# Optimization experiments

Hardware: AMD Instinct MI355X
Metric: run time of the kernel (lower is better)

The kernel has to match this reference:

```python
import jax, jax.numpy as jnp
import numpy as np
from functools import partial

WS = 11          # window size (safe for H=W=256)
SIGMA = 1.5
DATA_RANGE = 1.0
EPS = 1e-8


def _gaussian_window(ws: int, sigma: float, channels: int) -> jnp.ndarray:
    coords = jnp.arange(ws, dtype=jnp.float32) - ws // 2
    g = jnp.exp(-(coords ** 2) / (2.0 * sigma * sigma))
    g = g / (g.sum() + 1e-12)
    win2d = jnp.outer(g, g)                      # [ws, ws]
    # depthwise kernel: OIHW with O=C, I=1, feature_group_count=C
    return jnp.broadcast_to(win2d, (channels, 1, ws, ws))


def _depthwise_conv(x: jnp.ndarray, win: jnp.ndarray) -> jnp.ndarray:
    # x: [N, C, H, W]; same-padding depthwise Gaussian filter
    c = x.shape[1]
    pad = WS // 2
    return jax.lax.conv_general_dilated(
        x, win,
        window_strides=(1, 1),
        padding=[(pad, pad), (pad, pad)],
        dimension_numbers=('NCHW', 'OIHW', 'NCHW'),
        feature_group_count=c,
    )


def setup_inputs() -> dict:
    key = jax.random.key(0)
    k1, k2 = jax.random.split(key)
    shape = (8, 8, 3, 256, 256)  # [B, T, C, H, W]
    pred = jax.random.uniform(k1, shape, dtype=jnp.float32)
    target = jax.random.uniform(k2, shape, dtype=jnp.float32)
    return {"pred": pred, "target": target}


def reference(pred, target):
    pred = jnp.clip(pred.astype(jnp.float32), 0.0, 1.0)
    target = jnp.clip(target.astype(jnp.float32), 0.0, 1.0)
    B, T, C, H, W = pred.shape
    x = pred.reshape(B * T, C, H, W)
    y = target.reshape(B * T, C, H, W)

    win = _gaussian_window(WS, SIGMA, C)

    mu_x = _depthwise_conv(x, win)
    mu_y = _depthwise_conv(y, win)
    mu_x2 = mu_x * mu_x
    mu_y2 = mu_y * mu_y
    mu_xy = mu_x * mu_y

    sigma_x2 = jnp.maximum(_depthwise_conv(x * x, win) - mu_x2, 0.0)
    sigma_y2 = jnp.maximum(_depthwise_conv(y * y, win) - mu_y2, 0.0)
    sigma_xy = _depthwise_conv(x * y, win) - mu_xy

    C1 = (0.01 * DATA_RANGE) ** 2
    C2 = (0.03 * DATA_RANGE) ** 2
    num = (2.0 * mu_xy + C1) * (2.0 * sigma_xy + C2)
    den = (mu_x2 + mu_y2 + C1) * (sigma_x2 + sigma_y2 + C2)
    ssim_map = num / (den + EPS)
    ssim_map = jnp.nan_to_num(ssim_map, nan=0.0, posinf=0.0, neginf=0.0)
    return 1.0 - jnp.mean(ssim_map)
```

## Files before the change

kernel.cpp:

```cpp
#include <hip/hip_runtime.h>


typedef _Float16 h2 __attribute__((ext_vector_type(2)));
typedef __fp16 fp16v2 __attribute__((ext_vector_type(2)));

#define WSZ 11
#define RAD 5
#define IMH 256
#define IMW 256
#define BROWS 16
#define HROWS (BROWS + 2 * RAD)
#define NBANDS (IMH / BROWS)
#define NPLANES 192
#define NGRID (NPLANES * NBANDS)
#define WPB 4
#define RPW (BROWS / WPB)
#define NPIXF (192.0f * 256.0f * 256.0f)

#define GW0 0.001028381f
#define GW1 0.007598770f
#define GW2 0.036000770f
#define GW3 0.109360600f
#define GW4 0.213005700f
#define GW5 0.266011790f

__device__ __forceinline__ h2 pk_fma16(h2 a, h2 b, h2 c) {
    h2 d;
    asm("v_pk_fma_f16 %0, %1, %2, %3" : "=v"(d) : "v"(a), "v"(b), "v"(c));
    return d;
}
__device__ __forceinline__ h2 pk_mul16(h2 a, h2 b) {
    h2 d;
    asm("v_pk_mul_f16 %0, %1, %2" : "=v"(d) : "v"(a), "v"(b));
    return d;
}
__device__ __forceinline__ h2 pk_add16(h2 a, h2 b) {
    h2 d;
    asm("v_pk_add_f16 %0, %1, %2" : "=v"(d) : "v"(a), "v"(b));
    return d;
}
__device__ __forceinline__ h2 pk_min16(h2 a, h2 b) {
    h2 d;
    asm("v_pk_min_f16 %0, %1, %2" : "=v"(d) : "v"(a), "v"(b));
    return d;
}
__device__ __forceinline__ h2 pk_max16(h2 a, h2 b) {
    h2 d;
    asm("v_pk_max_f16 %0, %1, %2" : "=v"(d) : "v"(a), "v"(b));
    return d;
}

union H2U { h2 h; unsigned u; };
__device__ __forceinline__ unsigned h2u(h2 v) { H2U x; x.h = v; return x.u; }
__device__ __forceinline__ h2 u2h(unsigned v) { H2U x; x.u = v; return x.h; }

__device__ __forceinline__ h2 bperm(int idx, h2 v) {
    return u2h((unsigned)__builtin_amdgcn_ds_bpermute(idx, (int)h2u(v)));
}
__device__ __forceinline__ h2 albt(h2 hi, h2 lo) {
    return u2h(__builtin_amdgcn_alignbit(h2u(hi), h2u(lo), 16));
}

__device__ __forceinline__ h2 splat16(float s) {
    _Float16 t = (_Float16)s;
    return (h2){t, t};
}
__device__ __forceinline__ h2 zero16() { return (h2){(_Float16)0, (_Float16)0}; }

__device__ __forceinline__ h2 clip_pack(float a, float b, h2 Z, h2 O) {
    fp16v2 r = __builtin_amdgcn_cvt_pkrtz(a, b);
    h2 v = __builtin_bit_cast(h2, r);
    return pk_min16(pk_max16(v, Z), O);
}

__global__ __launch_bounds__(256, 4) void ssim_band_kernel(
    const float* __restrict__ pred,
    const float* __restrict__ targ,
    float* __restrict__ partial)
{
    const int tid = threadIdx.x;
    const int lane = tid & 63;
    const int wid = tid >> 6;
    const int blk = blockIdx.x;
    const int plane = blk >> 4;
    const int band = blk & 15;
    const int r0 = band * BROWS;

    const float4* __restrict__ pp =
        (const float4*)(pred + (size_t)plane * (IMH * IMW));
    const float4* __restrict__ tp =
        (const float4*)(targ + (size_t)plane * (IMH * IMW));

    const h2 W0 = splat16(GW0), W1 = splat16(GW1), W2 = splat16(GW2),
             W3 = splat16(GW3), W4 = splat16(GW4), W5 = splat16(GW5);
    const h2 wv16[WSZ] = {W0, W1, W2, W3, W4, W5, W4, W3, W2, W1, W0};
    const h2 M2 = splat16(-2.0f);
    const h2 Z16 = zero16();
    const h2 O16 = splat16(1.0f);

    __shared__ uint4 lds[HROWS * 64];
    __shared__ float wsum[WPB];

    for (int j = wid; j < HROWS; j += WPB) {
        const int r = r0 - RAD + j;
        const int rc = min(max(r, 0), IMH - 1);
        const bool oob = (r < 0) | (r >= IMH);
        const float4 a = pp[rc * 64 + lane];
        const float4 c = tp[rc * 64 + lane];
        const h2 x0 = clip_pack(a.x, a.y, Z16, O16);
        const h2 x1 = clip_pack(a.z, a.w, Z16, O16);
        const h2 y0 = clip_pack(c.x, c.y, Z16, O16);
        const h2 y1 = clip_pack(c.z, c.w, Z16, O16);
        const h2 s0 = pk_add16(x0, y0);
        const h2 s1 = pk_add16(x1, y1);
        const h2 d0 = pk_fma16(M2, y0, s0);
        const h2 d1 = pk_fma16(M2, y1, s1);
        uint4 w;
        w.x = oob ? 0u : h2u(s0);
        w.y = oob ? 0u : h2u(d0);
        w.z = oob ? 0u : h2u(s1);
        w.w = oob ? 0u : h2u(d1);
        lds[j * 64 + lane] = w;
    }
    __syncthreads();

    const int iu1 = (lane - 1) << 2;
    const int iu2 = (lane - 2) << 2;
    const int id1 = (lane + 1) << 2;
    const int id2 = (lane + 2) << 2;
    const bool mu1 = lane >= 1;
    const bool mu2 = lane >= 2;
    const bool md1 = lane <= 62;
    const bool md2 = lane <= 61;

    const float C1 = 1e-4f, C2 = 9e-4f;
    float lsum = 0.f;

#pragma unroll
    for (int i = 0; i < RPW; ++i) {
        const int jb = wid * RPW + i;

        h2 vd[4][2];
#pragma unroll
        for (int p = 0; p < 2; ++p) {
            vd[0][p] = zero16(); vd[1][p] = zero16();
            vd[2][p] = zero16(); vd[3][p] = zero16();
        }
#pragma unroll
        for (int k = 0; k < WSZ; ++k) {
            const uint4 v = lds[(jb + k) * 64 + lane];
            const h2 wk = wv16[k];
            const h2 sA = u2h(v.x), dA = u2h(v.y);
            const h2 sB = u2h(v.z), dB = u2h(v.w);
            h2 ws = pk_mul16(wk, sA);
            h2 wd = pk_mul16(wk, dA);
            vd[0][0] = pk_add16(vd[0][0], ws);
            vd[1][0] = pk_add16(vd[1][0], wd);
            vd[2][0] = pk_fma16(ws, sA, vd[2][0]);
            vd[3][0] = pk_fma16(wd, dA, vd[3][0]);
            ws = pk_mul16(wk, sB);
            wd = pk_mul16(wk, dB);
            vd[0][1] = pk_add16(vd[0][1], ws);
            vd[1][1] = pk_add16(vd[1][1], wd);
            vd[2][1] = pk_fma16(ws, sB, vd[2][1]);
            vd[3][1] = pk_fma16(wd, dB, vd[3][1]);
        }

        h2 hf[4][2];
#pragma unroll
        for (int ch = 0; ch < 4; ++ch) {
            const h2 H0 = vd[ch][0], H1 = vd[ch][1];
            h2 Gm3 = bperm(iu2, H1);
            h2 Gm2 = bperm(iu1, H0);
            h2 Gm1 = bperm(iu1, H1);
            h2 G2  = bperm(id1, H0);
            h2 G3  = bperm(id1, H1);
            h2 G4  = bperm(id2, H0);
            Gm3 = mu2 ? Gm3 : zero16();
            Gm2 = mu1 ? Gm2 : zero16();
            Gm1 = mu1 ? Gm1 : zero16();
            G2  = md1 ? G2  : zero16();
            G3  = md1 ? G3  : zero16();
            G4  = md2 ? G4  : zero16();
            const h2 P0  = albt(Gm2, Gm3);
            const h2 P1  = Gm2;
            const h2 P2  = albt(Gm1, Gm2);
            const h2 P3  = Gm1;
            const h2 P4  = albt(H0, Gm1);
            const h2 P5  = H0;
            const h2 P6  = albt(H1, H0);
            const h2 P7  = H1;
            const h2 P8  = albt(G2, H1);
            const h2 P9  = G2;
            const h2 P10 = albt(G3, G2);
            const h2 P11 = G3;
            const h2 P12 = albt(G4, G3);
            h2 a0 = pk_mul16(W0, P0);
            a0 = pk_fma16(W1, P1, a0);
            a0 = pk_fma16(W2, P2, a0);
            a0 = pk_fma16(W3, P3, a0);
            a0 = pk_fma16(W4, P4, a0);
            a0 = pk_fma16(W5, P5, a0);
            a0 = pk_fma16(W4, P6, a0);
            a0 = pk_fma16(W3, P7, a0);
            a0 = pk_fma16(W2, P8, a0);
            a0 = pk_fma16(W1, P9, a0);
            a0 = pk_fma16(W0, P10, a0);
            h2 a1 = pk_mul16(W0, P2);
            a1 = pk_fma16(W1, P3, a1);
            a1 = pk_fma16(W2, P4, a1);
            a1 = pk_fma16(W3, P5, a1);
            a1 = pk_fma16(W4, P6, a1);
            a1 = pk_fma16(W5, P7, a1);
            a1 = pk_fma16(W4, P8, a1);
            a1 = pk_fma16(W3, P9, a1);
            a1 = pk_fma16(W2, P10, a1);
            a1 = pk_fma16(W1, P11, a1);
            a1 = pk_fma16(W0, P12, a1);
            hf[ch][0] = a0;
            hf[ch][1] = a1;
        }

#pragma unroll
        for (int p = 0; p < 2; ++p) {
#pragma unroll
            for (int e = 0; e < 2; ++e) {
                const float ms = (float)hf[0][p][e];
                const float md = (float)hf[1][p][e];
                const float Ss = (float)hf[2][p][e];
                const float Sd = (float)hf[3][p][e];
                const float P = ms * ms, Q = md * md;
                const float mxy2 = 0.5f * (P - Q);
                const float m2s  = 0.5f * (P + Q);
                const float Ssum = 0.5f * (Ss + Sd);
                const float ssum = fmaxf(Ssum - m2s, 0.f);
                const float sxy2 = fmaf(0.5f, Ss - Sd, -mxy2);
                const float num = (mxy2 + C1) * (sxy2 + C2);
                const float den = fmaf(m2s + C1, ssum + C2, 1e-8f);
                lsum += num * __builtin_amdgcn_rcpf(den);
            }
        }
    }

#pragma unroll
    for (int off = 32; off > 0; off >>= 1)
        lsum += __shfl_xor(lsum, off, 64);

    if (lane == 0) wsum[wid] = lsum;
    __syncthreads();
    if (tid == 0)
        partial[blk] = wsum[0] + wsum[1] + wsum[2] + wsum[3];
}

__global__ __launch_bounds__(256) void ssim_finalize(
    const float* __restrict__ partial,
    float* __restrict__ out)
{
    __shared__ float wsum[4];
    const int t = threadIdx.x;
    float s = 0.f;
    for (int i = t; i < NGRID; i += 256) s += partial[i];
#pragma unroll
    for (int off = 32; off > 0; off >>= 1)
        s += __shfl_xor(s, off, 64);
    const int lane = t & 63, wv = t >> 6;
    if (lane == 0) wsum[wv] = s;
    __syncthreads();
    if (t == 0)
        out[0] = 1.0f - (wsum[0] + wsum[1] + wsum[2] + wsum[3]) / NPIXF;
}

extern "C" void kernel_launch(void* const* d_in, const int* in_sizes, int n_in,
                              void* d_out, int out_size, void* d_ws, size_t ws_size,
                              hipStream_t stream) {
    const float* pred = (const float*)d_in[0];
    const float* targ = (const float*)d_in[1];
    float* out = (float*)d_out;
    float* part = (float*)d_ws;

    ssim_band_kernel<<<NGRID, 256, 0, stream>>>(pred, targ, part);
    ssim_finalize<<<1, 256, 0, stream>>>(part, out);
}
```

Before: 142.5 us.

## Compute separable Gaussian convolutions with MFMA banded-matrix multiplies

Replaces the packed-FP16 vertical and horizontal 11-tap filters with 16x16x32 f16 MFMA operations against a banded Gaussian weight matrix generated per lane. Input rows are clipped, converted to sum/difference form and stored transposed in LDS. A vertical MFMA pass follows, its results are written back to LDS with zero padding, and a horizontal MFMA pass produces the four statistics. This moves the FMA-heavy stencil work from VALU onto matrix cores, at the cost of redundant zero multiplications, extra LDS traffic and transposes, and an additional barrier.

```diff
diff --git a/kernel.cpp b/kernel.cpp
--- a/kernel.cpp
+++ b/kernel.cpp
@@ -2,6 +2,9 @@
 
 
 typedef _Float16 h2 __attribute__((ext_vector_type(2)));
+typedef _Float16 half4 __attribute__((ext_vector_type(4)));
+typedef _Float16 half8 __attribute__((ext_vector_type(8)));
+typedef float f32x4 __attribute__((ext_vector_type(4)));
 typedef __fp16 fp16v2 __attribute__((ext_vector_type(2)));
 
 #define WSZ 11
@@ -9,20 +12,17 @@
 #define IMH 256
 #define IMW 256
 #define BROWS 16
-#define HROWS (BROWS + 2 * RAD)
 #define NBANDS (IMH / BROWS)
 #define NPLANES 192
 #define NGRID (NPLANES * NBANDS)
 #define WPB 4
-#define RPW (BROWS / WPB)
 #define NPIXF (192.0f * 256.0f * 256.0f)
 
-#define GW0 0.001028381f
-#define GW1 0.007598770f
-#define GW2 0.036000770f
-#define GW3 0.109360600f
-#define GW4 0.213005700f
-#define GW5 0.266011790f
+#define CSTRIDE 72
+#define INPLANE (256 * CSTRIDE)
+#define VROWSTRIDE 552
+#define VPLANE (16 * VROWSTRIDE)
+#define SMEM_BYTES 36864
 
 __device__ __forceinline__ h2 pk_fma16(h2 a, h2 b, h2 c) {
     h2 d;
@@ -52,14 +52,6 @@
 
 union H2U { h2 h; unsigned u; };
 __device__ __forceinline__ unsigned h2u(h2 v) { H2U x; x.h = v; return x.u; }
-__device__ __forceinline__ h2 u2h(unsigned v) { H2U x; x.u = v; return x.h; }
-
-__device__ __forceinline__ h2 bperm(int idx, h2 v) {
-    return u2h((unsigned)__builtin_amdgcn_ds_bpermute(idx, (int)h2u(v)));
-}
-__device__ __forceinline__ h2 albt(h2 hi, h2 lo) {
-    return u2h(__builtin_amdgcn_alignbit(h2u(hi), h2u(lo), 16));
-}
 
 __device__ __forceinline__ h2 splat16(float s) {
     _Float16 t = (_Float16)s;
@@ -71,6 +63,32 @@
     fp16v2 r = __builtin_amdgcn_cvt_pkrtz(a, b);
     h2 v = __builtin_bit_cast(h2, r);
     return pk_min16(pk_max16(v, Z), O);
+}
+
+__device__ __forceinline__ unsigned lo_pair(h2 a, h2 b) {
+    return __builtin_amdgcn_perm(h2u(b), h2u(a), 0x05040100u);
+}
+__device__ __forceinline__ unsigned hi_pair(h2 a, h2 b) {
+    return __builtin_amdgcn_perm(h2u(b), h2u(a), 0x07060302u);
+}
+
+__device__ __forceinline__ f32x4 mfma32(half8 a, half8 b, f32x4 c) {
+    return __builtin_amdgcn_mfma_f32_16x16x32_f16(a, b, c, 0, 0, 0);
+}
+
+__device__ __forceinline__ half8 cat8(half4 lo, half4 hi) {
+    half8 r;
+    r[0] = lo[0]; r[1] = lo[1]; r[2] = lo[2]; r[3] = lo[3];
+    r[4] = hi[0]; r[5] = hi[1]; r[6] = hi[2]; r[7] = hi[3];
+    return r;
+}
+
+__device__ __forceinline__ half4 sq4(half4 v) {
+    union { half4 v4; h2 h[2]; } u, r;
+    u.v4 = v;
+    r.h[0] = pk_mul16(u.h[0], u.h[0]);
+    r.h[1] = pk_mul16(u.h[1], u.h[1]);
+    return r.v4;
 }
 
 __global__ __launch_bounds__(256, 4) void ssim_band_kernel(
@@ -81,6 +99,8 @@
     const int tid = threadIdx.x;
     const int lane = tid & 63;
     const int wid = tid >> 6;
+    const int g = lane >> 4;
+    const int m = lane & 15;
     const int blk = blockIdx.x;
     const int plane = blk >> 4;
     const int band = blk & 15;
@@ -91,154 +111,144 @@
     const float4* __restrict__ tp =
         (const float4*)(targ + (size_t)plane * (IMH * IMW));
 
-    const h2 W0 = splat16(GW0), W1 = splat16(GW1), W2 = splat16(GW2),
-             W3 = splat16(GW3), W4 = splat16(GW4), W5 = splat16(GW5);
-    const h2 wv16[WSZ] = {W0, W1, W2, W3, W4, W5, W4, W3, W2, W1, W0};
+    __shared__ __align__(16) char smem[SMEM_BYTES];
+    __shared__ float wsum[WPB];
+
     const h2 M2 = splat16(-2.0f);
     const h2 Z16 = zero16();
     const h2 O16 = splat16(1.0f);
 
-    __shared__ uint4 lds[HROWS * 64];
-    __shared__ float wsum[WPB];
-
-    for (int j = wid; j < HROWS; j += WPB) {
-        const int r = r0 - RAD + j;
-        const int rc = min(max(r, 0), IMH - 1);
-        const bool oob = (r < 0) | (r >= IMH);
-        const float4 a = pp[rc * 64 + lane];
-        const float4 c = tp[rc * 64 + lane];
-        const h2 x0 = clip_pack(a.x, a.y, Z16, O16);
-        const h2 x1 = clip_pack(a.z, a.w, Z16, O16);
-        const h2 y0 = clip_pack(c.x, c.y, Z16, O16);
-        const h2 y1 = clip_pack(c.z, c.w, Z16, O16);
-        const h2 s0 = pk_add16(x0, y0);
-        const h2 s1 = pk_add16(x1, y1);
-        const h2 d0 = pk_fma16(M2, y0, s0);
-        const h2 d1 = pk_fma16(M2, y1, s1);
-        uint4 w;
-        w.x = oob ? 0u : h2u(s0);
-        w.y = oob ? 0u : h2u(d0);
-        w.z = oob ? 0u : h2u(s1);
-        w.w = oob ? 0u : h2u(d1);
-        lds[j * 64 + lane] = w;
-    }
-    __syncthreads();
-
-    const int iu1 = (lane - 1) << 2;
-    const int iu2 = (lane - 2) << 2;
-    const int id1 = (lane + 1) << 2;
-    const int id2 = (lane + 2) << 2;
-    const bool mu1 = lane >= 1;
-    const bool mu2 = lane >= 2;
-    const bool md1 = lane <= 62;
-    const bool md2 = lane <= 61;
+    half8 wf;
+    {
+#pragma unroll
+        for (int e = 0; e < 8; ++e) {
+            const int k = (e >> 2) * 16 + 4 * g + (e & 3);
+            const int dd = k - m;
+            const float t = (float)(dd - 5);
+            float w = 0.266011790f * exp2f(t * t * -0.32059890f);
+            if (dd < 0 || dd > 10) w = 0.f;
+            wf[e] = (_Float16)w;
+        }
+    }
+
+#pragma unroll
+    for (int q = 0; q < 2; ++q) {
+        const int kq = wid * 8 + q * 4;
+        h2 sA[4], sB[4], dA[4], dB[4];
+#pragma unroll
+        for (int dk = 0; dk < 4; ++dk) {
+            const int r = r0 - RAD + kq + dk;
+            const int rc = min(max(r, 0), IMH - 1);
+            const bool oob = (r < 0) | (r >= IMH);
+            const float4 a = pp[rc * 64 + lane];
+            const float4 c = tp[rc * 64 + lane];
+            const h2 x0 = clip_pack(a.x, a.y, Z16, O16);
+            const h2 x1 = clip_pack(a.z, a.w, Z16, O16);
+            const h2 y0 = clip_pack(c.x, c.y, Z16, O16);
+            const h2 y1 = clip_pack(c.z, c.w, Z16, O16);
+            h2 s0 = pk_add16(x0, y0);
+            h2 s1 = pk_add16(x1, y1);
+            h2 d0 = pk_fma16(M2, y0, s0);
+            h2 d1 = pk_fma16(M2, y1, s1);
+            sA[dk] = oob ? Z16 : s0;
+            sB[dk] = oob ? Z16 : s1;
+            dA[dk] = oob ? Z16 : d0;
+            dB[dk] = oob ? Z16 : d1;
+        }
+        char* const ws0 = smem + (size_t)(4 * lane) * CSTRIDE + kq * 2;
+        char* const wd0 = ws0 + INPLANE;
+        uint2 v;
+        v.x = lo_pair(sA[0], sA[1]); v.y = lo_pair(sA[2], sA[3]);
+        *(uint2*)(ws0 + 0 * CSTRIDE) = v;
+        v.x = hi_pair(sA[0], sA[1]); v.y = hi_pair(sA[2], sA[3]);
+        *(uint2*)(ws0 + 1 * CSTRIDE) = v;
+        v.x = lo_pair(sB[0], sB[1]); v.y = lo_pair(sB[2], sB[3]);
+        *(uint2*)(ws0 + 2 * CSTRIDE) = v;
+        v.x = hi_pair(sB[0], sB[1]); v.y = hi_pair(sB[2], sB[3]);
+        *(uint2*)(ws0 + 3 * CSTRIDE) = v;
+        v.x = lo_pair(dA[0], dA[1]); v.y = lo_pair(dA[2], dA[3]);
+        *(uint2*)(wd0 + 0 * CSTRIDE) = v;
+        v.x = hi_pair(dA[0], dA[1]); v.y = hi_pair(dA[2], dA[3]);
+        *(uint2*)(wd0 + 1 * CSTRIDE) = v;
+        v.x = lo_pair(dB[0], dB[1]); v.y = lo_pair(dB[2], dB[3]);
+        *(uint2*)(wd0 + 2 * CSTRIDE) = v;
+        v.x = hi_pair(dB[0], dB[1]); v.y = hi_pair(dB[2], dB[3]);
+        *(uint2*)(wd0 + 3 * CSTRIDE) = v;
+    }
+    __syncthreads();
+
+    f32x4 Dv[4][4];
+    const f32x4 z4 = {0.f, 0.f, 0.f, 0.f};
+#pragma unroll
+    for (int tt = 0; tt < 4; ++tt) {
+        const int c0 = (wid * 4 + tt) * 16;
+        const char* ps = smem + (size_t)(c0 + m) * CSTRIDE;
+        const char* pd = ps + INPLANE;
+        const half4 bs_lo = *(const half4*)(ps + 8 * g);
+        const half4 bs_hi = *(const half4*)(ps + 32 + 8 * g);
+        const half4 bd_lo = *(const half4*)(pd + 8 * g);
+        const half4 bd_hi = *(const half4*)(pd + 32 + 8 * g);
+        Dv[tt][0] = mfma32(wf, cat8(bs_lo, bs_hi), z4);
+        Dv[tt][1] = mfma32(wf, cat8(bd_lo, bd_hi), z4);
+        Dv[tt][2] = mfma32(wf, cat8(sq4(bs_lo), sq4(bs_hi)), z4);
+        Dv[tt][3] = mfma32(wf, cat8(sq4(bd_lo), sq4(bd_hi)), z4);
+    }
+    __syncthreads();
+
+#pragma unroll
+    for (int tt = 0; tt < 4; ++tt) {
+        const int c0 = (wid * 4 + tt) * 16;
+#pragma unroll
+        for (int ch = 0; ch < 4; ++ch) {
+            char* vp = smem + ch * VPLANE + (size_t)(5 + c0 + m) * 2;
+#pragma unroll
+            for (int r = 0; r < 4; ++r) {
+                *(__fp16*)(vp + (4 * g + r) * VROWSTRIDE) =
+                    (__fp16)Dv[tt][ch][r];
+            }
+        }
+    }
+#pragma unroll
+    for (int e = 0; e < 4; ++e) {
+        const int idx = tid * 4 + e;
+        const int ch = idx >> 8;
+        const int rem = idx & 255;
+        const int i = rem >> 4;
+        const int pc = rem & 15;
+        const int p = pc < 5 ? pc : pc + 256;
+        *(__fp16*)(smem + ch * VPLANE + i * VROWSTRIDE + p * 2) = (__fp16)0.f;
+    }
+    __syncthreads();
 
     const float C1 = 1e-4f, C2 = 9e-4f;
     float lsum = 0.f;
-
-#pragma unroll
-    for (int i = 0; i < RPW; ++i) {
-        const int jb = wid * RPW + i;
-
-        h2 vd[4][2];
-#pragma unroll
-        for (int p = 0; p < 2; ++p) {
-            vd[0][p] = zero16(); vd[1][p] = zero16();
-            vd[2][p] = zero16(); vd[3][p] = zero16();
-        }
-#pragma unroll
-        for (int k = 0; k < WSZ; ++k) {
-            const uint4 v = lds[(jb + k) * 64 + lane];
-            const h2 wk = wv16[k];
-            const h2 sA = u2h(v.x), dA = u2h(v.y);
-            const h2 sB = u2h(v.z), dB = u2h(v.w);
-            h2 ws = pk_mul16(wk, sA);
-            h2 wd = pk_mul16(wk, dA);
-            vd[0][0] = pk_add16(vd[0][0], ws);
-            vd[1][0] = pk_add16(vd[1][0], wd);
-            vd[2][0] = pk_fma16(ws, sA, vd[2][0]);
-            vd[3][0] = pk_fma16(wd, dA, vd[3][0]);
-            ws = pk_mul16(wk, sB);
-            wd = pk_mul16(wk, dB);
-            vd[0][1] = pk_add16(vd[0][1], ws);
-            vd[1][1] = pk_add16(vd[1][1], wd);
-            vd[2][1] = pk_fma16(ws, sB, vd[2][1]);
-            vd[3][1] = pk_fma16(wd, dB, vd[3][1]);
-        }
-
-        h2 hf[4][2];
+#pragma unroll
+    for (int tt = 0; tt < 4; ++tt) {
+        const int c0 = (wid * 4 + tt) * 16;
+        f32x4 D2[4];
 #pragma unroll
         for (int ch = 0; ch < 4; ++ch) {
-            const h2 H0 = vd[ch][0], H1 = vd[ch][1];
-            h2 Gm3 = bperm(iu2, H1);
-            h2 Gm2 = bperm(iu1, H0);
-            h2 Gm1 = bperm(iu1, H1);
-            h2 G2  = bperm(id1, H0);
-            h2 G3  = bperm(id1, H1);
-            h2 G4  = bperm(id2, H0);
-            Gm3 = mu2 ? Gm3 : zero16();
-            Gm2 = mu1 ? Gm2 : zero16();
-            Gm1 = mu1 ? Gm1 : zero16();
-            G2  = md1 ? G2  : zero16();
-            G3  = md1 ? G3  : zero16();
-            G4  = md2 ? G4  : zero16();
-            const h2 P0  = albt(Gm2, Gm3);
-            const h2 P1  = Gm2;
-            const h2 P2  = albt(Gm1, Gm2);
-            const h2 P3  = Gm1;
-            const h2 P4  = albt(H0, Gm1);
-            const h2 P5  = H0;
-            const h2 P6  = albt(H1, H0);
-            const h2 P7  = H1;
-            const h2 P8  = albt(G2, H1);
-            const h2 P9  = G2;
-            const h2 P10 = albt(G3, G2);
-            const h2 P11 = G3;
-            const h2 P12 = albt(G4, G3);
-            h2 a0 = pk_mul16(W0, P0);
-            a0 = pk_fma16(W1, P1, a0);
-            a0 = pk_fma16(W2, P2, a0);
-            a0 = pk_fma16(W3, P3, a0);
-            a0 = pk_fma16(W4, P4, a0);
-            a0 = pk_fma16(W5, P5, a0);
-            a0 = pk_fma16(W4, P6, a0);
-            a0 = pk_fma16(W3, P7, a0);
-            a0 = pk_fma16(W2, P8, a0);
-            a0 = pk_fma16(W1, P9, a0);
-            a0 = pk_fma16(W0, P10, a0);
-            h2 a1 = pk_mul16(W0, P2);
-            a1 = pk_fma16(W1, P3, a1);
-            a1 = pk_fma16(W2, P4, a1);
-            a1 = pk_fma16(W3, P5, a1);
-            a1 = pk_fma16(W4, P6, a1);
-            a1 = pk_fma16(W5, P7, a1);
-            a1 = pk_fma16(W4, P8, a1);
-            a1 = pk_fma16(W3, P9, a1);
-            a1 = pk_fma16(W2, P10, a1);
-            a1 = pk_fma16(W1, P11, a1);
-            a1 = pk_fma16(W0, P12, a1);
-            hf[ch][0] = a0;
-            hf[ch][1] = a1;
-        }
-
-#pragma unroll
-        for (int p = 0; p < 2; ++p) {
-#pragma unroll
-            for (int e = 0; e < 2; ++e) {
-                const float ms = (float)hf[0][p][e];
-                const float md = (float)hf[1][p][e];
-                const float Ss = (float)hf[2][p][e];
-                const float Sd = (float)hf[3][p][e];
-                const float P = ms * ms, Q = md * md;
-                const float mxy2 = 0.5f * (P - Q);
-                const float m2s  = 0.5f * (P + Q);
-                const float Ssum = 0.5f * (Ss + Sd);
-                const float ssum = fmaxf(Ssum - m2s, 0.f);
-                const float sxy2 = fmaf(0.5f, Ss - Sd, -mxy2);
-                const float num = (mxy2 + C1) * (sxy2 + C2);
-                const float den = fmaf(m2s + C1, ssum + C2, 1e-8f);
-                lsum += num * __builtin_amdgcn_rcpf(den);
-            }
+            const char* vb = smem + ch * VPLANE + (size_t)m * VROWSTRIDE
+                           + (size_t)c0 * 2;
+            const half4 a_lo = *(const half4*)(vb + 8 * g);
+            const half4 a_hi = *(const half4*)(vb + 32 + 8 * g);
+            D2[ch] = mfma32(cat8(a_lo, a_hi), wf, z4);
+        }
+#pragma unroll
+        for (int r = 0; r < 4; ++r) {
+            const float ms = D2[0][r];
+            const float md = D2[1][r];
+            const float Ss = D2[2][r];
+            const float Sd = D2[3][r];
+            const float P = ms * ms, Q = md * md;
+            const float mxy2 = 0.5f * (P - Q);
+            const float m2s  = 0.5f * (P + Q);
+            const float Ssum = 0.5f * (Ss + Sd);
+            const float ssum = fmaxf(Ssum - m2s, 0.f);
+            const float sxy2 = fmaf(0.5f, Ss - Sd, -mxy2);
+            const float num = (mxy2 + C1) * (sxy2 + C2);
+            const float den = fmaf(m2s + C1, ssum + C2, 1e-8f);
+            lsum += num * __builtin_amdgcn_rcpf(den);
         }
     }
 
```

Result: faster. 128.0 us (-10.2%).
